# Performance work log

Hardware: AMD Instinct MI355X
Metric: run time of the kernel (lower is better)

The kernel has to match this reference:

```python
import jax, jax.numpy as jnp
import numpy as np

HEADS = 8
TQ, QH, QW = 4, 16, 16
TK, KH, KW = 4, 16, 16
DIM = 64


def setup_inputs() -> dict:
    key = jax.random.key(0)
    k1, k2, k3, k4, k5 = jax.random.split(key, 5)
    return {
        "query": jax.random.normal(k1, (4, HEADS, TQ * QH * QW, DIM), dtype=jnp.float32),
        "scores": jax.random.normal(k2, (4, HEADS, TQ * QH * QW, TK * KH * KW), dtype=jnp.float32),
        "height_embeddings": jax.random.normal(k3, (2 * (max(QH, KH) - 1) + 1, DIM), dtype=jnp.float32),
        "width_embeddings": jax.random.normal(k4, (2 * (max(QW, KW) - 1) + 1, DIM), dtype=jnp.float32),
        "time_embeddings": jax.random.normal(k5, (2 * (max(TQ, TK) - 1) + 1, DIM), dtype=jnp.float32),
    }


def _rel_dist(q_n, k_n):
    # matches torch: ratios are both 1 when q_n == k_n
    q_ratio = round(max(k_n / q_n, 1.0))
    k_ratio = round(max(q_n / k_n, 1.0))
    d = jnp.arange(q_n)[:, None] * q_ratio - jnp.arange(k_n)[None, :] * k_ratio
    return d + (k_n - 1) * k_ratio  # [q_n, k_n] int indices


def reference(query, scores, height_embeddings, width_embeddings, time_embeddings):
    Rh = height_embeddings[_rel_dist(QH, KH)]  # [QH, KH, DIM]
    Rw = width_embeddings[_rel_dist(QW, KW)]   # [QW, KW, DIM]
    Rt = time_embeddings[_rel_dist(TQ, TK)]    # [TQ, TK, DIM]

    q = query.reshape(-1, HEADS, TQ, QH, QW, DIM)
    rel_h = jnp.einsum('bNthwc,hkc->bNthwk', q, Rh)  # [B,N,T,H,W,KH]
    rel_w = jnp.einsum('bNthwc,wkc->bNthwk', q, Rw)  # [B,N,T,H,W,KW]
    rel_t = jnp.einsum('bNthwc,tkc->bNthwk', q, Rt)  # [B,N,T,H,W,TK]

    s = scores.reshape(-1, HEADS, TQ, QH, QW, TK, KH, KW)
    s = (s
         + rel_h[:, :, :, :, :, None, :, None]
         + rel_w[:, :, :, :, :, None, None, :]
         + rel_t[:, :, :, :, :, :, None, None])
    return s.reshape(-1, HEADS, TQ * QH * QW, TK * KH * KW)
```

## Files before the change

kernel.cpp:

```cpp
#include <hip/hip_runtime.h>

#define NHEADS 8
#define TQ 4
#define QH 16
#define QW 16
#define TK 4
#define KH 16
#define KW 16
#define DIM 64
#define BATCH 4

#define ROWS (BATCH * NHEADS * TQ * QH * QW)
#define RPB 16

typedef float f4 __attribute__((ext_vector_type(4)));

__global__ __launch_bounds__(256) void relpos16_kernel(
    const float* __restrict__ query,
    const float* __restrict__ scores,
    const float* __restrict__ hemb,
    const float* __restrict__ wemb,
    const float* __restrict__ temb,
    float* __restrict__ out)
{
    const int tid  = threadIdx.x;
    const int row0 = blockIdx.x * RPB;
    const int pos  = row0 & 1023;
    const int t = pos >> 8;
    const int h = (pos >> 4) & 15;

    __shared__ float rel[RPB][36];

    for (int d = tid; d < RPB * 36; d += 256) {
        const int r = d / 36;
        const int j = d - r * 36;
        const float* emb;
        int e;
        if (j < 16)      { emb = hemb; e = h - j + 15; }
        else if (j < 32) { emb = wemb; e = r - (j - 16) + 15; }
        else             { emb = temb; e = t - (j - 32) + 3; }
        const float4* e4 = (const float4*)(emb + (size_t)e * DIM);
        const float4* q4 = (const float4*)(query + (size_t)(row0 + r) * DIM);
        float acc = 0.f;
#pragma unroll
        for (int c = 0; c < DIM / 4; ++c) {
            float4 qv = q4[c];
            float4 ev = e4[c];
            acc += qv.x * ev.x + qv.y * ev.y + qv.z * ev.z + qv.w * ev.w;
        }
        rel[r][j] = acc;
    }
    __syncthreads();

    const int tk  = tid >> 6;
    const int kh  = (tid >> 2) & 15;
    const int kw0 = (tid & 3) << 2;

    const f4* sc4 = (const f4*)(scores + (size_t)row0 * 1024);
    f4*       o4  = (f4*)(out + (size_t)row0 * 1024);

    f4 cur = sc4[tid];
#pragma unroll
    for (int r = 0; r < RPB; ++r) {
        f4 nxt;
        if (r < RPB - 1) nxt = sc4[(r + 1) * 256 + tid];
        const float a = rel[r][kh] + rel[r][32 + tk];
        f4 o;
        o.x = cur.x + a + rel[r][16 + kw0 + 0];
        o.y = cur.y + a + rel[r][16 + kw0 + 1];
        o.z = cur.z + a + rel[r][16 + kw0 + 2];
        o.w = cur.w + a + rel[r][16 + kw0 + 3];
        __builtin_nontemporal_store(o, o4 + r * 256 + tid);
        cur = nxt;
    }
}

extern "C" void kernel_launch(void* const* d_in, const int* in_sizes, int n_in,
                              void* d_out, int out_size, void* d_ws, size_t ws_size,
                              hipStream_t stream) {
    const float* query  = (const float*)d_in[0];
    const float* scores = (const float*)d_in[1];
    const float* hemb   = (const float*)d_in[2];
    const float* wemb   = (const float*)d_in[3];
    const float* temb   = (const float*)d_in[4];
    float* out = (float*)d_out;

    relpos16_kernel<<<dim3(ROWS / RPB), dim3(256), 0, stream>>>(
        query, scores, hemb, wemb, temb, out);
}
```

Before: 276.7 us.

## Stage query and embeddings in LDS, issue all score loads before rel compute

Copies the block's query rows and the needed height, width and time embedding rows into padded shared memory, so the dot products read from LDS rather than repeatedly from global memory. Each wave now owns four rows and issues all 16 of its score loads, marked nontemporal, before computing the relative terms. This hides the rel computation behind the score fetch latency. It adds about 30KB of LDS per block, which may limit occupancy, and the prefetched scores raise register pressure.

```diff
diff --git a/kernel.cpp b/kernel.cpp
--- a/kernel.cpp
+++ b/kernel.cpp
@@ -12,10 +12,11 @@
 
 #define ROWS (BATCH * NHEADS * TQ * QH * QW)
 #define RPB 16
+#define EST 68
 
 typedef float f4 __attribute__((ext_vector_type(4)));
 
-__global__ __launch_bounds__(256) void relpos16_kernel(
+__global__ __launch_bounds__(256) void relpos_stage_kernel(
     const float* __restrict__ query,
     const float* __restrict__ scores,
     const float* __restrict__ hemb,
@@ -24,54 +25,86 @@
     float* __restrict__ out)
 {
     const int tid  = threadIdx.x;
+    const int lane = tid & 63;
+    const int wv   = tid >> 6;
     const int row0 = blockIdx.x * RPB;
     const int pos  = row0 & 1023;
     const int t = pos >> 8;
     const int h = (pos >> 4) & 15;
 
-    __shared__ float rel[RPB][36];
+    __shared__ float lds_q[RPB][EST];
+    __shared__ float lds_h[16][EST];
+    __shared__ float lds_w[31][EST];
+    __shared__ float lds_t[4][EST];
+    __shared__ float rel[RPB][40];
 
-    for (int d = tid; d < RPB * 36; d += 256) {
-        const int r = d / 36;
-        const int j = d - r * 36;
-        const float* emb;
-        int e;
-        if (j < 16)      { emb = hemb; e = h - j + 15; }
-        else if (j < 32) { emb = wemb; e = r - (j - 16) + 15; }
-        else             { emb = temb; e = t - (j - 32) + 3; }
-        const float4* e4 = (const float4*)(emb + (size_t)e * DIM);
-        const float4* q4 = (const float4*)(query + (size_t)(row0 + r) * DIM);
-        float acc = 0.f;
-#pragma unroll
-        for (int c = 0; c < DIM / 4; ++c) {
-            float4 qv = q4[c];
-            float4 ev = e4[c];
-            acc += qv.x * ev.x + qv.y * ev.y + qv.z * ev.z + qv.w * ev.w;
+    {
+        const f4* sq = (const f4*)(query + (size_t)row0 * DIM);
+        const f4* sh = (const f4*)(hemb + (size_t)h * DIM);
+        const f4* sw = (const f4*)wemb;
+        const f4* st = (const f4*)(temb + (size_t)t * DIM);
+        {
+            const int r = tid >> 4, c = tid & 15;
+            *(f4*)&lds_q[r][4 * c] = sq[tid];
+            *(f4*)&lds_h[r][4 * c] = sh[tid];
+            *(f4*)&lds_w[r][4 * c] = sw[tid];
         }
-        rel[r][j] = acc;
+        if (tid < 240) {
+            const int k = 256 + tid;
+            *(f4*)&lds_w[k >> 4][4 * (k & 15)] = sw[k];
+        }
+        if (tid < 64)
+            *(f4*)&lds_t[tid >> 4][4 * (tid & 15)] = st[tid];
     }
     __syncthreads();
 
-    const int tk  = tid >> 6;
-    const int kh  = (tid >> 2) & 15;
-    const int kw0 = (tid & 3) << 2;
+    const size_t rbase = (size_t)(row0 + wv * 4) * 1024;
+    f4 s[4][4];
+#pragma unroll
+    for (int r = 0; r < 4; ++r) {
+        const f4* sp = (const f4*)(scores + rbase + (size_t)r * 1024);
+#pragma unroll
+        for (int i = 0; i < 4; ++i)
+            s[r][i] = __builtin_nontemporal_load(sp + lane + 64 * i);
+    }
 
-    const f4* sc4 = (const f4*)(scores + (size_t)row0 * 1024);
-    f4*       o4  = (f4*)(out + (size_t)row0 * 1024);
+#pragma unroll
+    for (int d0 = 0; d0 < 144; d0 += 64) {
+        const int d = d0 + lane;
+        if (d < 144) {
+            const int rl  = d / 36;
+            const int j   = d - rl * 36;
+            const int row = wv * 4 + rl;
+            const float* ep;
+            if (j < 16)      ep = &lds_h[15 - j][0];
+            else if (j < 32) ep = &lds_w[row - (j - 16) + 15][0];
+            else             ep = &lds_t[3 - (j - 32)][0];
+            const float* qp = &lds_q[row][0];
+            float acc = 0.f;
+#pragma unroll
+            for (int c = 0; c < 16; ++c) {
+                f4 qv = *(const f4*)(qp + 4 * c);
+                f4 ev = *(const f4*)(ep + 4 * c);
+                acc += qv.x * ev.x + qv.y * ev.y + qv.z * ev.z + qv.w * ev.w;
+            }
+            rel[row][j] = acc;
+        }
+    }
 
-    f4 cur = sc4[tid];
+    const int kh  = lane >> 2;
+    const int kw0 = (lane << 2) & 15;
 #pragma unroll
-    for (int r = 0; r < RPB; ++r) {
-        f4 nxt;
-        if (r < RPB - 1) nxt = sc4[(r + 1) * 256 + tid];
-        const float a = rel[r][kh] + rel[r][32 + tk];
-        f4 o;
-        o.x = cur.x + a + rel[r][16 + kw0 + 0];
-        o.y = cur.y + a + rel[r][16 + kw0 + 1];
-        o.z = cur.z + a + rel[r][16 + kw0 + 2];
-        o.w = cur.w + a + rel[r][16 + kw0 + 3];
-        __builtin_nontemporal_store(o, o4 + r * 256 + tid);
-        cur = nxt;
+    for (int r = 0; r < 4; ++r) {
+        const int row = wv * 4 + r;
+        const float hv = rel[row][kh];
+        const f4 tv  = *(const f4*)&rel[row][32];
+        const f4 wv4 = *(const f4*)&rel[row][16 + kw0];
+        f4* op = (f4*)(out + rbase + (size_t)r * 1024);
+#pragma unroll
+        for (int i = 0; i < 4; ++i) {
+            f4 o = s[r][i] + (hv + tv[i]) + wv4;
+            __builtin_nontemporal_store(o, op + lane + 64 * i);
+        }
     }
 }
 
@@ -85,6 +118,6 @@
     const float* temb   = (const float*)d_in[4];
     float* out = (float*)d_out;
 
-    relpos16_kernel<<<dim3(ROWS / RPB), dim3(256), 0, stream>>>(
+    relpos_stage_kernel<<<dim3(ROWS / RPB), dim3(256), 0, stream>>>(
         query, scores, hemb, wemb, temb, out);
 }
```

Measured after the change: 236.6 us (median of 2 runs). -14.5%, faster.
